# Kernel optimization log

Hardware: AMD Instinct MI355X
Metric: run time of the kernel (lower is better)

Reference implementation:

```python
import jax, jax.numpy as jnp
import numpy as np

NEG_SLOPE = 0.1

def mlp(x, w1, b1, w2, b2):
    # MLP(sizes): Linear -> LeakyReLU(0.1) -> Linear
    return jax.nn.leaky_relu(x @ w1 + b1, NEG_SLOPE) @ w2 + b2

def _seg_mean(vals, idx, n):
    s = jax.ops.segment_sum(vals, idx, num_segments=n)
    cnt = jax.ops.segment_sum(jnp.ones((vals.shape[0],), vals.dtype), idx, num_segments=n)
    return s / jnp.maximum(cnt, 1.0)[:, None]

def setup_inputs() -> dict:
    key = jax.random.key(0)
    ks = iter(jax.random.split(key, 40))
    N, F, H, E = 100000, 64, 128, 800000
    Ha = H // 2  # hidden_dim/2 = 64
    def lin(k, i, o):
        k1, k2 = jax.random.split(k)
        return (jax.random.normal(k1, (i, o), jnp.float32) * (1.0 / np.sqrt(i)),
                jax.random.normal(k2, (o,), jnp.float32) * 0.01)
    inp = {}
    inp['feat'] = jax.random.normal(next(ks), (N, F), jnp.float32)
    inp['pi_feat'] = jax.random.normal(next(ks), (N, 4), jnp.float32)
    inp['level'] = jax.random.uniform(next(ks), (N, 1), jnp.float32)
    inp['bit_position'] = jax.random.uniform(next(ks), (E, 1), jnp.float32)
    inp['is_po'] = jax.random.randint(next(ks), (N,), 0, 2, jnp.int32)
    inp['is_module'] = jax.random.randint(next(ks), (N,), 0, 2, jnp.int32)
    inp['src_m'] = jax.random.randint(next(ks), (E,), 0, N, jnp.int32)
    inp['dst_m'] = jax.random.randint(next(ks), (E,), 0, N, jnp.int32)
    inp['src_g'] = jax.random.randint(next(ks), (E,), 0, N, jnp.int32)
    inp['dst_g'] = jax.random.randint(next(ks), (E,), 0, N, jnp.int32)
    # mlp_pi: 4 -> H/2 -> H
    inp['pi_w1'], inp['pi_b1'] = lin(next(ks), 4, Ha)
    inp['pi_w2'], inp['pi_b2'] = lin(next(ks), Ha, H)
    # mlp_neigh_module: H + F + 1 -> H/2 -> H
    inp['nm_w1'], inp['nm_b1'] = lin(next(ks), H + F + 1, Ha)
    inp['nm_w2'], inp['nm_b2'] = lin(next(ks), Ha, H)
    # mlp_neigh_gate: H + F -> H/2 -> H
    inp['ng_w1'], inp['ng_b1'] = lin(next(ks), H + F, Ha)
    inp['ng_w2'], inp['ng_b2'] = lin(next(ks), Ha, H)
    # mlp_global: 1 -> H/2 -> H
    inp['g_w1'], inp['g_b1'] = lin(next(ks), 1, Ha)
    inp['g_w2'], inp['g_b2'] = lin(next(ks), Ha, H)
    # mlp_out: 2H -> H -> 1
    inp['o_w1'], inp['o_b1'] = lin(next(ks), 2 * H, H)
    inp['o_w2'], inp['o_b2'] = lin(next(ks), H, 1)
    return inp

def reference(feat, pi_feat, level, bit_position,
              pi_w1, pi_b1, pi_w2, pi_b2,
              nm_w1, nm_b1, nm_w2, nm_b2,
              ng_w1, ng_b1, ng_w2, ng_b2,
              g_w1, g_b1, g_w2, g_b2,
              o_w1, o_b1, o_w2, o_b2,
              is_po, is_module, src_m, dst_m, src_g, dst_g):
    N = feat.shape[0]
    # PI init embedding (mlp_pi)
    h0 = mlp(pi_feat, pi_w1, pi_b1, pi_w2, pi_b2)            # [N, H]
    # module-edge message passing: m = src h, pos = bit_position; mean reduce
    m = h0[src_m]                                            # [E, H] irregular gather
    neigh_m = _seg_mean(m, dst_m, N)                         # [N, H]
    pos_m = _seg_mean(bit_position, dst_m, N)                # [N, 1]
    # nodes_func_module, agg_choice==0: cat(neigh, pos, feat) -> mlp_neigh_module
    h_m = mlp(jnp.concatenate([neigh_m, pos_m, feat], axis=1), nm_w1, nm_b1, nm_w2, nm_b2)
    # gate-edge message passing
    neigh_g = _seg_mean(h0[src_g], dst_g, N)                 # [N, H]
    h_g = mlp(jnp.concatenate([neigh_g, feat], axis=1), ng_w1, ng_b1, ng_w2, ng_b2)
    # ReLU on non-PO nodes only
    keep = (is_po != 1)[:, None]
    h_m = jnp.where(keep, jax.nn.relu(h_m), h_m)
    h_g = jnp.where(keep, jax.nn.relu(h_g), h_g)
    # per-node-type update (hetero apply_nodes)
    h = jnp.where((is_module == 1)[:, None], h_m, h_g)       # [N, H]
    # global branch + readout
    hg = mlp(level, g_w1, g_b1, g_w2, g_b2)                  # [N, H]
    out = mlp(jnp.concatenate([h, hg], axis=1), o_w1, o_b1, o_w2, o_b2)  # [N, 1]
    return out
```

## Files before the change

kernel.cpp:

```cpp
#include <hip/hip_runtime.h>

typedef __bf16 bf16x8 __attribute__((ext_vector_type(8)));
typedef float f32x4 __attribute__((ext_vector_type(4)));
typedef unsigned short u16;
typedef unsigned int u32;
typedef unsigned long long u64;

__device__ __forceinline__ u16 f2b(float f) {
  return __builtin_bit_cast(u16, (__bf16)f);
}
__device__ __forceinline__ float b2f_lo(u32 pk) {
  return __builtin_bit_cast(float, pk << 16);
}
__device__ __forceinline__ float b2f_hi(u32 pk) {
  return __builtin_bit_cast(float, pk & 0xffff0000u);
}
__device__ __forceinline__ float leaky(float x) { return x > 0.f ? x : 0.1f * x; }
__device__ __forceinline__ f32x4 mfma16(bf16x8 a, bf16x8 b, f32x4 c) {
  return __builtin_amdgcn_mfma_f32_16x16x32_bf16(a, b, c, 0, 0, 0);
}

#define P64 72
#define P128 136
#define CAP 16
#define RSTRIDE 32

__global__ __launch_bounds__(256) void k_prep(
    const float* nm_w1, const float* ng_w1, const float* nm_w2, const float* ng_w2,
    const float* o_w1, const float* o_b1, const float* g_w2, const float* g_b2,
    const float* pi_w2, const float* pi_b2, const int* is_module,
    u16* wt_yc, float* bias_y, u16* wt_f1m, u16* wt_f1g, float* w_pos,
    u16* wt2m, u16* wt2g, u16* wt_oh, u16* gt, float* bp, u32* mbits, int N) {
  int i = blockIdx.x * 256 + threadIdx.x;
  if (i < 9216) {
    int ty = i / 4608, rem = i % 4608, n = rem / P64, k = rem % P64;
    float v = 0.f;
    if (k < 64) {
      const float* w1 = ty ? ng_w1 : nm_w1;
      for (int t = 0; t < 128; t++) v += pi_w2[k * 128 + t] * w1[t * 64 + n];
    }
    wt_yc[i] = f2b(v);
    return;
  }
  i -= 9216;
  if (i < 128) {
    int ty = i >> 6, n = i & 63;
    const float* w1 = ty ? ng_w1 : nm_w1;
    float v = 0.f;
    for (int t = 0; t < 128; t++) v += pi_b2[t] * w1[t * 64 + n];
    bias_y[i] = v;
    return;
  }
  i -= 128;
  if (i < 4608) {
    int n = i / P64, k = i % P64;
    wt_f1m[i] = f2b(k < 64 ? nm_w1[(129 + k) * 64 + n] : 0.f);
    return;
  }
  i -= 4608;
  if (i < 4608) {
    int n = i / P64, k = i % P64;
    wt_f1g[i] = f2b(k < 64 ? ng_w1[(128 + k) * 64 + n] : 0.f);
    return;
  }
  i -= 4608;
  if (i < 64) { w_pos[i] = nm_w1[128 * 64 + i]; return; }
  i -= 64;
  if (i < 9216) {
    int n = i / P64, k = i % P64;
    wt2m[i] = f2b(k < 64 ? nm_w2[k * 128 + n] : 0.f);
    return;
  }
  i -= 9216;
  if (i < 9216) {
    int n = i / P64, k = i % P64;
    wt2g[i] = f2b(k < 64 ? ng_w2[k * 128 + n] : 0.f);
    return;
  }
  i -= 9216;
  if (i < 17408) {
    int n = i / P128, k = i % P128;
    wt_oh[i] = f2b(k < 128 ? o_w1[k * 128 + n] : 0.f);
    return;
  }
  i -= 17408;
  if (i < 9216) {
    int n = i / P64, k = i % P64;
    float v = 0.f;
    if (k < 64)
      for (int t = 0; t < 128; t++) v += g_w2[k * 128 + t] * o_w1[(128 + t) * 128 + n];
    gt[i] = f2b(v);
    return;
  }
  i -= 9216;
  if (i < 128) {
    float s = o_b1[i];
    for (int t = 0; t < 128; t++) s += g_b2[t] * o_w1[(128 + t) * 128 + i];
    bp[i] = s;
    return;
  }
  i -= 128;
  {
    int n = i;
    int lane = threadIdx.x & 63;
    bool v = (n < N) && (is_module[n] == 1);
    u64 b = __ballot(v);
    if (lane == 0 && n < N) mbits[n >> 5] = (u32)b;
    if (lane == 32 && n < N) mbits[n >> 5] = (u32)(b >> 32);
  }
}

__global__ void k_scatter(const int* src_m, const int* dst_m, const int* src_g,
                          const int* dst_g, const u32* mbits, const float* bitpos,
                          int* rec, u64* spill, int* spillcnt, int E) {
  int e0 = (blockIdx.x * 256 + threadIdx.x) * 2;
#pragma unroll
  for (int j = 0; j < 2; j++) {
    int e = e0 + j;
    if (e < E) {
      int d = dst_m[e];
      if ((mbits[d >> 5] >> (d & 31)) & 1) {
        int c = atomicAdd(&rec[d * RSTRIDE], 1);
        int s = src_m[e];
        float bpv = bitpos[e];
        if (c < CAP) {
          int bp12 = (int)(bpv * 4096.f);
          if (bp12 > 4095) bp12 = 4095;
          rec[(size_t)d * RSTRIDE + 2 + c] = (s << 12) | bp12;
        } else {
          int p = atomicAdd(spillcnt, 1);
          spill[p] = ((u64)(u32)d << 32) | (u32)s;
          atomicAdd((float*)&rec[d * RSTRIDE + 1], bpv);
        }
      }
    } else if (e < 2 * E) {
      int d = dst_g[e - E];
      if (!((mbits[d >> 5] >> (d & 31)) & 1)) {
        int c = atomicAdd(&rec[d * RSTRIDE], 1);
        int s = src_g[e - E];
        if (c < CAP) {
          rec[(size_t)d * RSTRIDE + 2 + c] = s << 12;
        } else {
          int p = atomicAdd(spillcnt, 1);
          spill[p] = ((u64)(u32)d << 32) | (u32)s;
        }
      }
    }
  }
}

__global__ __launch_bounds__(512) void k_pre(const float* pf, const float* feat,
                                             const float* pi_w1, const float* pi_b1,
                                             const u16* wt_yc_g, const float* bias_y,
                                             const u16* wt_f1m_g, const u16* wt_f1g_g,
                                             const float* nm_b1, const float* ng_b1,
                                             const u32* mbits,
                                             u16* y0, u16* f1, int N) {
  __shared__ __align__(16) u16 wyc[2][64 * P64];
  __shared__ __align__(16) u16 wf[2][64 * P64];
  __shared__ __align__(16) u16 tbuf[8][16 * P64];
  for (int i = threadIdx.x; i < 2304; i += 512) {
    ((u32*)wyc[0])[i] = ((const u32*)wt_yc_g)[i];
    ((u32*)wyc[1])[i] = ((const u32*)wt_yc_g)[2304 + i];
    ((u32*)wf[0])[i] = ((const u32*)wt_f1m_g)[i];
    ((u32*)wf[1])[i] = ((const u32*)wt_f1g_g)[i];
  }

  int lane = threadIdx.x & 63, wv = threadIdx.x >> 6;
  int lid = lane & 15, q = lane >> 4;

  bf16x8 w1f[4];
#pragma unroll
  for (int nt = 0; nt < 4; nt++) {
    bf16x8 f;
#pragma unroll
    for (int j = 0; j < 8; j++) {
      int k = q * 8 + j;
      f[j] = (__bf16)((k < 4) ? pi_w1[k * 64 + nt * 16 + lid] : 0.f);
    }
    w1f[nt] = f;
  }
  __syncthreads();

  int nbat = (N + 15) >> 4;
  for (int b0 = blockIdx.x * 8; b0 < nbat; b0 += gridDim.x * 8) {
    int b = b0 + wv;
    int batch = b < nbat ? b : nbat - 1;
    int id = batch * 16 + lid;
    if (id >= N) id = N - 1;

    bf16x8 a;
#pragma unroll
    for (int j = 0; j < 8; j++)
      a[j] = (__bf16)((q == 0 && j < 4) ? pf[(size_t)id * 4 + j] : 0.f);
    f32x4 z1[4];
#pragma unroll
    for (int nt = 0; nt < 4; nt++) {
      f32x4 c = {0.f, 0.f, 0.f, 0.f};
      z1[nt] = mfma16(a, w1f[nt], c);
    }
    __syncthreads();
#pragma unroll
    for (int nt = 0; nt < 4; nt++) {
      float bb = pi_b1[nt * 16 + lid];
#pragma unroll
      for (int r = 0; r < 4; r++)
        tbuf[wv][(q * 4 + r) * P64 + nt * 16 + lid] = f2b(leaky(z1[nt][r] + bb));
    }
    __syncthreads();
    bf16x8 a20 = *(const bf16x8*)&tbuf[wv][lid * P64 + q * 8];
    bf16x8 a21 = *(const bf16x8*)&tbuf[wv][lid * P64 + 32 + q * 8];

    int idr_[4];
#pragma unroll
    for (int r = 0; r < 4; r++) {
      int ii = batch * 16 + q * 4 + r;
      idr_[r] = ii < N ? ii : N - 1;
    }

#pragma unroll
    for (int ty = 0; ty < 2; ty++) {
#pragma unroll
      for (int nt = 0; nt < 4; nt++) {
        f32x4 c = {0.f, 0.f, 0.f, 0.f};
        c = mfma16(a20, *(const bf16x8*)&wyc[ty][(nt * 16 + lid) * P64 + q * 8], c);
        c = mfma16(a21, *(const bf16x8*)&wyc[ty][(nt * 16 + lid) * P64 + 32 + q * 8], c);
        float by = bias_y[ty * 64 + nt * 16 + lid];
#pragma unroll
        for (int r = 0; r < 4; r++)
          y0[(size_t)idr_[r] * 128 + ty * 64 + nt * 16 + lid] = f2b(c[r] + by);
      }
    }

    bf16x8 af[2];
#pragma unroll
    for (int kt = 0; kt < 2; kt++) {
      const float4* p = (const float4*)(feat + (size_t)id * 64 + kt * 32 + q * 8);
      float4 xa = p[0], xb = p[1];
      bf16x8 f;
      f[0] = (__bf16)xa.x; f[1] = (__bf16)xa.y; f[2] = (__bf16)xa.z; f[3] = (__bf16)xa.w;
      f[4] = (__bf16)xb.x; f[5] = (__bf16)xb.y; f[6] = (__bf16)xb.z; f[7] = (__bf16)xb.w;
      af[kt] = f;
    }
#pragma unroll
    for (int nt = 0; nt < 4; nt++) {
      f32x4 cm = {0.f, 0.f, 0.f, 0.f}, cg = {0.f, 0.f, 0.f, 0.f};
#pragma unroll
      for (int kt = 0; kt < 2; kt++) {
        cm = mfma16(af[kt], *(const bf16x8*)&wf[0][(nt * 16 + lid) * P64 + kt * 32 + q * 8], cm);
        cg = mfma16(af[kt], *(const bf16x8*)&wf[1][(nt * 16 + lid) * P64 + kt * 32 + q * 8], cg);
      }
      float bm = nm_b1[nt * 16 + lid], bg = ng_b1[nt * 16 + lid];
#pragma unroll
      for (int r = 0; r < 4; r++) {
        int idr = idr_[r];
        bool mod = (mbits[idr >> 5] >> (idr & 31)) & 1;
        f1[(size_t)idr * 64 + nt * 16 + lid] = f2b(mod ? cm[r] + bm : cg[r] + bg);
      }
    }
  }
}

__global__ __launch_bounds__(256) void k_gather(const u16* y0, const int* rec,
                                                const u64* spill, const int* spillcnt,
                                                const u32* mbits, const u16* f1,
                                                const float* w_pos, u16* z1a, int N) {
  int n = (blockIdx.x * 256 + threadIdx.x) >> 6;
  int lane = threadIdx.x & 63;
  if (n >= N) return;
  bool mod = (mbits[n >> 5] >> (n & 31)) & 1;
  int sub = lane >> 5, l32 = lane & 31;
  int rv = (lane < 18) ? rec[(size_t)n * RSTRIDE + lane] : 0;
  int cnt = __shfl(rv, 0);
  float pspill = __builtin_bit_cast(float, __shfl(rv, 1));
  int inl = cnt < CAP ? cnt : CAP;
  float myb = 0.f;
  if (mod && lane >= 2 && lane < 18 && (lane - 2) < inl)
    myb = (float)(rv & 4095) * (1.f / 4096.f);
  const u32* yrow = (const u32*)y0;
  int halfo = mod ? 0 : 32;
  float a0 = 0.f, a1 = 0.f;
  for (int j = 0; j < inl; j += 2) {
    int e2 = j + sub;
    if (e2 < inl) {
      int s = (int)(((u32)__shfl(rv, 2 + e2)) >> 12);
      u32 pk = yrow[(size_t)s * 64 + halfo + l32];
      a0 += b2f_lo(pk);
      a1 += b2f_hi(pk);
    }
  }
  if (cnt > CAP) {
    int sc = *spillcnt;
    for (int base = 0; base < sc; base += 64) {
      int i = base + lane;
      u64 ent = (i < sc) ? spill[i] : 0xffffffffffffffffull;
      bool m = ((int)(ent >> 32) == n);
      u64 bal = __ballot(m);
      int slo = (int)(ent & 0xffffffffu);
      while (bal) {
        int l = __ffsll((long long)bal) - 1;
        bal &= bal - 1;
        int s = __shfl(slo, l);
        if (sub == 0) {
          u32 pk = yrow[(size_t)s * 64 + halfo + l32];
          a0 += b2f_lo(pk);
          a1 += b2f_hi(pk);
        }
      }
    }
  }
  a0 += __shfl_xor(a0, 32);
  a1 += __shfl_xor(a1, 32);
#pragma unroll
  for (int off = 1; off < 64; off <<= 1) myb += __shfl_xor(myb, off);
  float psum = pspill + myb;
  float inv = 1.f / (float)(cnt > 1 ? cnt : 1);
  if (sub == 0) {
    u32 fp = ((const u32*)f1)[(size_t)n * 32 + l32];
    float z0 = a0 * inv + b2f_lo(fp);
    float z1v = a1 * inv + b2f_hi(fp);
    if (mod) {
      float pm = psum * inv;
      float2 wp = ((const float2*)w_pos)[l32];
      z0 += pm * wp.x;
      z1v += pm * wp.y;
    }
    ((u32*)z1a)[(size_t)n * 32 + l32] = (u32)f2b(leaky(z0)) | ((u32)f2b(leaky(z1v)) << 16);
  }
}

__global__ __launch_bounds__(512) void k_tail(const u16* z1a, const u16* wt2m_g,
                                              const u16* wt2g_g, const float* nm_b2,
                                              const float* ng_b2, const u32* mbits,
                                              const int* is_po, const float* level,
                                              const float* g_w1, const float* g_b1,
                                              const u16* wt_oh_g, const u16* gt_g,
                                              const float* bp_g, const float* o_w2,
                                              const float* o_b2, float* out, int N) {
  __shared__ __align__(16) u16 w2[2][128 * P64];
  __shared__ __align__(16) u16 wt_oh[128 * P128];
  __shared__ __align__(16) u16 gt[128 * P64];
  __shared__ __align__(16) u16 tbuf[8][16 * P128];
  for (int i = threadIdx.x; i < 128 * P64 / 2; i += 512) {
    ((u32*)w2[0])[i] = ((const u32*)wt2m_g)[i];
    ((u32*)w2[1])[i] = ((const u32*)wt2g_g)[i];
    ((u32*)gt)[i] = ((const u32*)gt_g)[i];
  }
  for (int i = threadIdx.x; i < 128 * P128 / 2; i += 512)
    ((u32*)wt_oh)[i] = ((const u32*)wt_oh_g)[i];

  int lane = threadIdx.x & 63, wv = threadIdx.x >> 6;
  int lid = lane & 15, q = lane >> 4;
  int nbat = (N + 15) >> 4;

  float gw[2][8], gb[2][8];
#pragma unroll
  for (int kt = 0; kt < 2; kt++)
#pragma unroll
    for (int j = 0; j < 8; j++) {
      int k = kt * 32 + q * 8 + j;
      gw[kt][j] = g_w1[k];
      gb[kt][j] = g_b1[k];
    }
  float w2o[8], bpv[8];
#pragma unroll
  for (int nt = 0; nt < 8; nt++) {
    w2o[nt] = o_w2[nt * 16 + lid];
    bpv[nt] = bp_g[nt * 16 + lid];
  }
  float b2m[8], b2g[8];
#pragma unroll
  for (int nt = 0; nt < 8; nt++) {
    b2m[nt] = nm_b2[nt * 16 + lid];
    b2g[nt] = ng_b2[nt * 16 + lid];
  }
  float ob2 = o_b2[0];
  __syncthreads();

  for (int b0 = blockIdx.x * 8; b0 < nbat; b0 += gridDim.x * 8) {
    int b = b0 + wv;
    int batch = b < nbat ? b : nbat - 1;
    int id = batch * 16 + lid;
    if (id >= N) id = N - 1;

    bf16x8 a0 = *(const bf16x8*)(z1a + (size_t)id * 64 + q * 8);
    bf16x8 a1 = *(const bf16x8*)(z1a + (size_t)id * 64 + 32 + q * 8);
    bool mod_[4], kp_[4];
#pragma unroll
    for (int r = 0; r < 4; r++) {
      int ii = batch * 16 + q * 4 + r;
      if (ii >= N) ii = N - 1;
      mod_[r] = (mbits[ii >> 5] >> (ii & 31)) & 1;
      kp_[r] = (is_po[ii] != 1);
    }
    __syncthreads();
#pragma unroll
    for (int nt = 0; nt < 8; nt++) {
      f32x4 cm = {0.f, 0.f, 0.f, 0.f}, cg = {0.f, 0.f, 0.f, 0.f};
      cm = mfma16(a0, *(const bf16x8*)&w2[0][(nt * 16 + lid) * P64 + q * 8], cm);
      cm = mfma16(a1, *(const bf16x8*)&w2[0][(nt * 16 + lid) * P64 + 32 + q * 8], cm);
      cg = mfma16(a0, *(const bf16x8*)&w2[1][(nt * 16 + lid) * P64 + q * 8], cg);
      cg = mfma16(a1, *(const bf16x8*)&w2[1][(nt * 16 + lid) * P64 + 32 + q * 8], cg);
#pragma unroll
      for (int r = 0; r < 4; r++) {
        float v = mod_[r] ? cm[r] + b2m[nt] : cg[r] + b2g[nt];
        if (kp_[r]) v = fmaxf(v, 0.f);
        tbuf[wv][(q * 4 + r) * P128 + nt * 16 + lid] = f2b(v);
      }
    }
    __syncthreads();

    bf16x8 ah[4];
#pragma unroll
    for (int kt = 0; kt < 4; kt++)
      ah[kt] = *(const bf16x8*)&tbuf[wv][lid * P128 + kt * 32 + q * 8];
    float lv = level[id];
    bf16x8 ag[2];
#pragma unroll
    for (int kt = 0; kt < 2; kt++)
#pragma unroll
      for (int j = 0; j < 8; j++)
        ag[kt][j] = (__bf16)leaky(lv * gw[kt][j] + gb[kt][j]);

    f32x4 accv[8];
#pragma unroll
    for (int nt = 0; nt < 8; nt++) {
      f32x4 c = {0.f, 0.f, 0.f, 0.f};
#pragma unroll
      for (int kt = 0; kt < 4; kt++)
        c = mfma16(ah[kt], *(const bf16x8*)&wt_oh[(nt * 16 + lid) * P128 + kt * 32 + q * 8], c);
#pragma unroll
      for (int kt = 0; kt < 2; kt++)
        c = mfma16(ag[kt], *(const bf16x8*)&gt[(nt * 16 + lid) * P64 + kt * 32 + q * 8], c);
      accv[nt] = c;
    }
    float p[4];
#pragma unroll
    for (int r = 0; r < 4; r++) {
      float s = 0.f;
#pragma unroll
      for (int nt = 0; nt < 8; nt++) s += leaky(accv[nt][r] + bpv[nt]) * w2o[nt];
      p[r] = s;
    }
#pragma unroll
    for (int r = 0; r < 4; r++)
#pragma unroll
      for (int off = 1; off < 16; off <<= 1) p[r] += __shfl_xor(p[r], off, 16);
    if (lid == 0) {
#pragma unroll
      for (int r = 0; r < 4; r++) {
        int idr = batch * 16 + q * 4 + r;
        if (idr >= N) idr = N - 1;
        out[idr] = p[r] + ob2;
      }
    }
  }
}

extern "C" void kernel_launch(void* const* d_in, const int* in_sizes, int n_in,
                              void* d_out, int out_size, void* d_ws, size_t ws_size,
                              hipStream_t stream) {
  const float* feat = (const float*)d_in[0];
  const float* pi_feat = (const float*)d_in[1];
  const float* level = (const float*)d_in[2];
  const float* bitpos = (const float*)d_in[3];
  const int* is_po = (const int*)d_in[4];
  const int* is_module = (const int*)d_in[5];
  const int* src_m = (const int*)d_in[6];
  const int* dst_m = (const int*)d_in[7];
  const int* src_g = (const int*)d_in[8];
  const int* dst_g = (const int*)d_in[9];
  const float* pi_w1 = (const float*)d_in[10];
  const float* pi_b1 = (const float*)d_in[11];
  const float* pi_w2 = (const float*)d_in[12];
  const float* pi_b2 = (const float*)d_in[13];
  const float* nm_w1 = (const float*)d_in[14];
  const float* nm_b1 = (const float*)d_in[15];
  const float* nm_w2 = (const float*)d_in[16];
  const float* nm_b2 = (const float*)d_in[17];
  const float* ng_w1 = (const float*)d_in[18];
  const float* ng_b1 = (const float*)d_in[19];
  const float* ng_w2 = (const float*)d_in[20];
  const float* ng_b2 = (const float*)d_in[21];
  const float* g_w1 = (const float*)d_in[22];
  const float* g_b1 = (const float*)d_in[23];
  const float* g_w2 = (const float*)d_in[24];
  const float* g_b2 = (const float*)d_in[25];
  const float* o_w1 = (const float*)d_in[26];
  const float* o_b1 = (const float*)d_in[27];
  const float* o_w2 = (const float*)d_in[28];
  const float* o_b2 = (const float*)d_in[29];

  int N = in_sizes[0] / 64;
  int E = in_sizes[3];

  char* ws = (char*)d_ws;
  size_t off = 0;
  auto alloc = [&](size_t bytes) {
    char* p = ws + off;
    off += (bytes + 255) & ~(size_t)255;
    return p;
  };
  int* rec = (int*)alloc(((size_t)N * RSTRIDE + 64) * 4);
  int* spillcnt = (int*)alloc(16);
  size_t zero_bytes = off;
  u64* spill = (u64*)alloc((size_t)2 * E * 8);
  u32* mbits = (u32*)alloc((size_t)((N + 31) / 32) * 4);
  u16* y0 = (u16*)alloc((size_t)N * 128 * 2);
  u16* f1 = (u16*)alloc((size_t)N * 64 * 2);
  u16* z1a = (u16*)alloc((size_t)N * 64 * 2);
  u16* wt_yc = (u16*)alloc(9216 * 2);
  float* bias_y = (float*)alloc(128 * 4);
  u16* wt_f1m = (u16*)alloc(4608 * 2);
  u16* wt_f1g = (u16*)alloc(4608 * 2);
  float* w_pos = (float*)alloc(64 * 4);
  u16* wt2m = (u16*)alloc(9216 * 2);
  u16* wt2g = (u16*)alloc(9216 * 2);
  u16* wt_oh = (u16*)alloc(17408 * 2);
  u16* gt = (u16*)alloc(9216 * 2);
  float* bp = (float*)alloc(128 * 4);

  hipMemsetAsync(rec, 0, zero_bytes, stream);

  int prep_items = 63808 + ((N + 63) & ~63);
  k_prep<<<(prep_items + 255) / 256, 256, 0, stream>>>(
      nm_w1, ng_w1, nm_w2, ng_w2, o_w1, o_b1, g_w2, g_b2, pi_w2, pi_b2, is_module,
      wt_yc, bias_y, wt_f1m, wt_f1g, w_pos, wt2m, wt2g, wt_oh, gt, bp, mbits, N);

  k_scatter<<<(2 * E + 511) / 512, 256, 0, stream>>>(src_m, dst_m, src_g, dst_g,
                                                     mbits, bitpos, rec, spill,
                                                     spillcnt, E);

  k_pre<<<512, 512, 0, stream>>>(
      pi_feat, feat, pi_w1, pi_b1, wt_yc, bias_y, wt_f1m, wt_f1g,
      nm_b1, ng_b1, mbits, y0, f1, N);

  k_gather<<<(N * 64 + 255) / 256, 256, 0, stream>>>(
      y0, rec, spill, spillcnt, mbits, f1, w_pos, z1a, N);

  k_tail<<<256, 512, 0, stream>>>(z1a, wt2m, wt2g, nm_b2, ng_b2, mbits, is_po,
                                  level, g_w1, g_b1, wt_oh, gt, bp, o_w2, o_b2,
                                  (float*)d_out, N);
}
```

Before: 282.4 us.

## Fuse edge scatter and node pre-MLP into one block-specialized kernel

Merges the separate edge-scatter kernel and the per-node pre-MLP kernel into one launch. The first 256 blocks run a grid-stride loop over edges doing the atomic bucketing, and the remaining 256 blocks run the MLP work. The goal is to run the two independent stages concurrently and remove a launch boundary. In exchange, the scatter blocks now reserve the MLP kernel's large shared-memory footprint, and there are far fewer scatter threads in flight, which may reduce how well atomic latency is hidden.

New measurement: 280.3 us. About the same (-0.7%).

```diff
diff --git a/kernel.cpp b/kernel.cpp
--- a/kernel.cpp
+++ b/kernel.cpp
@@ -24,6 +24,9 @@
 #define P128 136
 #define CAP 16
 #define RSTRIDE 32
+
+#define SBLK 256
+#define PBLK 256
 
 __global__ __launch_bounds__(256) void k_prep(
     const float* nm_w1, const float* ng_w1, const float* nm_w2, const float* ng_w2,
@@ -110,55 +113,59 @@
   }
 }
 
-__global__ void k_scatter(const int* src_m, const int* dst_m, const int* src_g,
-                          const int* dst_g, const u32* mbits, const float* bitpos,
-                          int* rec, u64* spill, int* spillcnt, int E) {
-  int e0 = (blockIdx.x * 256 + threadIdx.x) * 2;
-#pragma unroll
-  for (int j = 0; j < 2; j++) {
-    int e = e0 + j;
-    if (e < E) {
-      int d = dst_m[e];
-      if ((mbits[d >> 5] >> (d & 31)) & 1) {
-        int c = atomicAdd(&rec[d * RSTRIDE], 1);
-        int s = src_m[e];
-        float bpv = bitpos[e];
-        if (c < CAP) {
-          int bp12 = (int)(bpv * 4096.f);
-          if (bp12 > 4095) bp12 = 4095;
-          rec[(size_t)d * RSTRIDE + 2 + c] = (s << 12) | bp12;
-        } else {
-          int p = atomicAdd(spillcnt, 1);
-          spill[p] = ((u64)(u32)d << 32) | (u32)s;
-          atomicAdd((float*)&rec[d * RSTRIDE + 1], bpv);
-        }
-      }
-    } else if (e < 2 * E) {
-      int d = dst_g[e - E];
-      if (!((mbits[d >> 5] >> (d & 31)) & 1)) {
-        int c = atomicAdd(&rec[d * RSTRIDE], 1);
-        int s = src_g[e - E];
-        if (c < CAP) {
-          rec[(size_t)d * RSTRIDE + 2 + c] = s << 12;
-        } else {
-          int p = atomicAdd(spillcnt, 1);
-          spill[p] = ((u64)(u32)d << 32) | (u32)s;
-        }
-      }
-    }
-  }
-}
-
-__global__ __launch_bounds__(512) void k_pre(const float* pf, const float* feat,
-                                             const float* pi_w1, const float* pi_b1,
-                                             const u16* wt_yc_g, const float* bias_y,
-                                             const u16* wt_f1m_g, const u16* wt_f1g_g,
-                                             const float* nm_b1, const float* ng_b1,
-                                             const u32* mbits,
-                                             u16* y0, u16* f1, int N) {
+__global__ __launch_bounds__(512) void k_mid(
+    const int* src_m, const int* dst_m, const int* src_g, const int* dst_g,
+    const u32* mbits, const float* bitpos, int* rec, u64* spill, int* spillcnt,
+    int E,
+    const float* pf, const float* feat, const float* pi_w1, const float* pi_b1,
+    const u16* wt_yc_g, const float* bias_y, const u16* wt_f1m_g, const u16* wt_f1g_g,
+    const float* nm_b1, const float* ng_b1, u16* y0, u16* f1, int N) {
   __shared__ __align__(16) u16 wyc[2][64 * P64];
   __shared__ __align__(16) u16 wf[2][64 * P64];
   __shared__ __align__(16) u16 tbuf[8][16 * P64];
+
+  if (blockIdx.x < SBLK) {
+    int tid = blockIdx.x * 512 + threadIdx.x;
+    for (int vt = tid; vt < E; vt += SBLK * 512) {
+      int e0 = vt * 2;
+#pragma unroll
+      for (int j = 0; j < 2; j++) {
+        int e = e0 + j;
+        if (e < E) {
+          int d = dst_m[e];
+          if ((mbits[d >> 5] >> (d & 31)) & 1) {
+            int c = atomicAdd(&rec[d * RSTRIDE], 1);
+            int s = src_m[e];
+            float bpv = bitpos[e];
+            if (c < CAP) {
+              int bp12 = (int)(bpv * 4096.f);
+              if (bp12 > 4095) bp12 = 4095;
+              rec[(size_t)d * RSTRIDE + 2 + c] = (s << 12) | bp12;
+            } else {
+              int p = atomicAdd(spillcnt, 1);
+              spill[p] = ((u64)(u32)d << 32) | (u32)s;
+              atomicAdd((float*)&rec[d * RSTRIDE + 1], bpv);
+            }
+          }
+        } else if (e < 2 * E) {
+          int d = dst_g[e - E];
+          if (!((mbits[d >> 5] >> (d & 31)) & 1)) {
+            int c = atomicAdd(&rec[d * RSTRIDE], 1);
+            int s = src_g[e - E];
+            if (c < CAP) {
+              rec[(size_t)d * RSTRIDE + 2 + c] = s << 12;
+            } else {
+              int p = atomicAdd(spillcnt, 1);
+              spill[p] = ((u64)(u32)d << 32) | (u32)s;
+            }
+          }
+        }
+      }
+    }
+    return;
+  }
+
+  int pb = blockIdx.x - SBLK;
   for (int i = threadIdx.x; i < 2304; i += 512) {
     ((u32*)wyc[0])[i] = ((const u32*)wt_yc_g)[i];
     ((u32*)wyc[1])[i] = ((const u32*)wt_yc_g)[2304 + i];
@@ -183,7 +190,7 @@
   __syncthreads();
 
   int nbat = (N + 15) >> 4;
-  for (int b0 = blockIdx.x * 8; b0 < nbat; b0 += gridDim.x * 8) {
+  for (int b0 = pb * 8; b0 < nbat; b0 += PBLK * 8) {
     int b = b0 + wv;
     int batch = b < nbat ? b : nbat - 1;
     int id = batch * 16 + lid;
@@ -527,13 +534,10 @@
       nm_w1, ng_w1, nm_w2, ng_w2, o_w1, o_b1, g_w2, g_b2, pi_w2, pi_b2, is_module,
       wt_yc, bias_y, wt_f1m, wt_f1g, w_pos, wt2m, wt2g, wt_oh, gt, bp, mbits, N);
 
-  k_scatter<<<(2 * E + 511) / 512, 256, 0, stream>>>(src_m, dst_m, src_g, dst_g,
-                                                     mbits, bitpos, rec, spill,
-                                                     spillcnt, E);
-
-  k_pre<<<512, 512, 0, stream>>>(
+  k_mid<<<SBLK + PBLK, 512, 0, stream>>>(
+      src_m, dst_m, src_g, dst_g, mbits, bitpos, rec, spill, spillcnt, E,
       pi_feat, feat, pi_w1, pi_b1, wt_yc, bias_y, wt_f1m, wt_f1g,
-      nm_b1, ng_b1, mbits, y0, f1, N);
+      nm_b1, ng_b1, y0, f1, N);
 
   k_gather<<<(N * 64 + 255) / 256, 256, 0, stream>>>(
       y0, rec, spill, spillcnt, mbits, f1, w_pos, z1a, N);
```
